# Performance work log

Hardware: AMD Instinct MI355X
Metric: run time of the kernel (lower is better)

Reference implementation:

```python
import jax, jax.numpy as jnp
import numpy as np

N_DST = 100000


def setup_inputs() -> dict:
    key = jax.random.key(0)
    ks = jax.random.split(key, 12)
    R, Ns, E, Din, H = 3, 100000, 1000000, 128, 64
    return {
        "dst_feat": jax.random.normal(ks[0], (N_DST, Din), jnp.float32),
        "neigh_feats": jax.random.normal(ks[1], (R, Ns, Din), jnp.float32),
        "Wt": jax.random.normal(ks[2], (R + 1, Din, H), jnp.float32) * 0.05,
        "bt": jnp.zeros((R + 1, H), jnp.float32),
        "attn_l": jax.random.normal(ks[3], (R, H), jnp.float32) * 0.1,
        "attn_r": jax.random.normal(ks[4], (R, H), jnp.float32) * 0.1,
        "W1": jax.random.normal(ks[5], (H, 128), jnp.float32) * 0.1,
        "b1": jnp.zeros((128,), jnp.float32),
        "w2": jax.random.normal(ks[6], (128, 1), jnp.float32) * 0.1,
        "src_idx": jax.random.randint(ks[7], (R, E), 0, Ns, jnp.int32),
        "dst_idx": jax.random.randint(ks[8], (R, E), 0, N_DST, jnp.int32),
    }


def _gat_relation(h_src, h_dst, al, ar, src, dst):
    # el/er: per-node attention logits (dot with attn vectors)
    el = h_src @ al  # [Ns]
    er = h_dst @ ar  # [Nd]
    e = jax.nn.leaky_relu(el[src] + er[dst], 0.01)  # [E]
    # edge softmax per destination node (segment softmax)
    m = jax.ops.segment_max(e, dst, num_segments=N_DST)
    a = jnp.exp(e - m[dst])
    s = jax.ops.segment_sum(a, dst, num_segments=N_DST)
    a = a / s[dst]
    # weighted aggregation: sum_e a_e * h_src[src_e]
    out = jax.ops.segment_sum(h_src[src] * a[:, None], dst, num_segments=N_DST)
    return jax.nn.elu(out)


def reference(dst_feat, neigh_feats, Wt, bt, attn_l, attn_r, W1, b1, w2, src_idx, dst_idx):
    R = neigh_feats.shape[0]
    h_dst = dst_feat @ Wt[0] + bt[0]  # weight_T[0]
    z_r = []
    for r in range(R):
        h_src = neigh_feats[r] @ Wt[r + 1] + bt[r + 1]
        z_r.append(_gat_relation(h_src, h_dst, attn_l[r], attn_r[r], src_idx[r], dst_idx[r]))
    z_r = jnp.stack(z_r, axis=1)  # [N, R, D]
    # semantic attention
    w = (jnp.tanh(z_r @ W1 + b1) @ w2).mean(axis=0)  # [R, 1]
    a_w = jax.nn.softmax(w, axis=0)  # softmax over relations
    z = (z_r * a_w[None]).sum(axis=1)  # [N, D]
    return z
```

## Files before the change

kernel.cpp:

```cpp
#include <hip/hip_runtime.h>
#include <hip/hip_fp16.h>

#define N_DST 100000
#define DIN 128
#define HDIM 64
#define RREL 3
#define NE 1000000

#define NBKT_REL 196
#define NBKT (RREL * NBKT_REL)
#define NSEG (RREL * N_DST)
#define EDGE_CHUNK 16384
#define NBLK_BIN ((RREL * NE + EDGE_CHUNK - 1) / EDGE_CHUNK)

typedef _Float16 f16x8 __attribute__((ext_vector_type(8)));
typedef float f32x4 __attribute__((ext_vector_type(4)));

__global__ __launch_bounds__(256) void k_gemm(
    const float* __restrict__ dst_feat, const float* __restrict__ neigh,
    const float* __restrict__ Wt, const float* __restrict__ bt,
    const float* __restrict__ attn_l, const float* __restrict__ attn_r,
    __half* __restrict__ h16, float* __restrict__ el, float* __restrict__ er) {
  const int RB = (N_DST + 127) / 128;
  int mat = blockIdx.x / RB;
  int row0 = (blockIdx.x % RB) * 128;
  const float* A = (mat == 0) ? dst_feat : (neigh + (size_t)(mat - 1) * N_DST * DIN);
  const float* W = Wt + (size_t)mat * DIN * HDIM;
  const float* b = bt + mat * HDIM;

  __shared__ __align__(16) unsigned char lds[48 * 1024];
  unsigned char* ldsA = lds;
  unsigned char* ldsW = lds + 32768;

  int tid = threadIdx.x;

#pragma unroll
  for (int i = 0; i < 8; i++) {
    int s = tid + 256 * i;
    int row = s >> 4;
    int kb = s & 15;
    int gr = row0 + row;
    if (gr >= N_DST) gr = N_DST - 1;
    const float* ap = A + (size_t)gr * DIN + kb * 8;
    float4 v0 = *(const float4*)ap;
    float4 v1 = *(const float4*)(ap + 4);
    f16x8 hv;
    hv[0] = (_Float16)v0.x; hv[1] = (_Float16)v0.y;
    hv[2] = (_Float16)v0.z; hv[3] = (_Float16)v0.w;
    hv[4] = (_Float16)v1.x; hv[5] = (_Float16)v1.y;
    hv[6] = (_Float16)v1.z; hv[7] = (_Float16)v1.w;
    *(f16x8*)(ldsA + row * 256 + ((kb * 16) ^ ((row & 7) << 4))) = hv;
  }

  {
    int col = tid & 63;
    int kq = tid >> 6;
    const float* wp = W + (size_t)(kq * 32) * HDIM + col;
    float wr[32];
#pragma unroll
    for (int m = 0; m < 32; m++) wr[m] = wp[(size_t)m * HDIM];
#pragma unroll
    for (int m8 = 0; m8 < 4; m8++) {
      f16x8 hv;
#pragma unroll
      for (int j = 0; j < 8; j++) hv[j] = (_Float16)wr[m8 * 8 + j];
      int byt = kq * 64 + m8 * 16;
      *(f16x8*)(ldsW + col * 256 + (byt ^ ((col & 7) << 4))) = hv;
    }
  }
  __syncthreads();

  int w = tid >> 6;
  int l = tid & 63;
  int li = l & 15;
  int hi = l >> 4;
  f32x4 acc[2][4] = {};
#pragma unroll
  for (int ks = 0; ks < 4; ks++) {
    int kbyte = ks * 64 + hi * 16;
    f16x8 af[2], bf[4];
#pragma unroll
    for (int rt = 0; rt < 2; rt++) {
      int row = w * 32 + rt * 16 + li;
      af[rt] = *(f16x8*)(ldsA + row * 256 + (kbyte ^ ((row & 7) << 4)));
    }
#pragma unroll
    for (int ct = 0; ct < 4; ct++) {
      int col = ct * 16 + li;
      bf[ct] = *(f16x8*)(ldsW + col * 256 + (kbyte ^ ((col & 7) << 4)));
    }
#pragma unroll
    for (int rt = 0; rt < 2; rt++)
#pragma unroll
      for (int ct = 0; ct < 4; ct++)
        acc[rt][ct] = __builtin_amdgcn_mfma_f32_16x16x32_f16(af[rt], bf[ct], acc[rt][ct], 0, 0, 0);
  }

  float bv[4];
#pragma unroll
  for (int ct = 0; ct < 4; ct++) bv[ct] = b[ct * 16 + li];
#pragma unroll
  for (int rt = 0; rt < 2; rt++)
#pragma unroll
    for (int ct = 0; ct < 4; ct++)
#pragma unroll
      for (int j = 0; j < 4; j++) acc[rt][ct][j] += bv[ct];

  if (mat == 0) {
#pragma unroll
    for (int r = 0; r < RREL; r++) {
      float av[4];
#pragma unroll
      for (int ct = 0; ct < 4; ct++) av[ct] = attn_r[r * HDIM + ct * 16 + li];
#pragma unroll
      for (int rt = 0; rt < 2; rt++) {
        float p[4];
#pragma unroll
        for (int j = 0; j < 4; j++)
          p[j] = acc[rt][0][j] * av[0] + acc[rt][1][j] * av[1] +
                 acc[rt][2][j] * av[2] + acc[rt][3][j] * av[3];
#pragma unroll
        for (int o = 1; o < 16; o <<= 1)
#pragma unroll
          for (int j = 0; j < 4; j++) p[j] += __shfl_xor(p[j], o);
        if (li == 0) {
#pragma unroll
          for (int j = 0; j < 4; j++) {
            int gr = row0 + w * 32 + rt * 16 + hi * 4 + j;
            if (gr < N_DST) er[r * N_DST + gr] = p[j];
          }
        }
      }
    }
  } else {
    int r = mat - 1;
    float av[4];
#pragma unroll
    for (int ct = 0; ct < 4; ct++) av[ct] = attn_l[r * HDIM + ct * 16 + li];
#pragma unroll
    for (int rt = 0; rt < 2; rt++) {
      float p[4];
#pragma unroll
      for (int j = 0; j < 4; j++)
        p[j] = acc[rt][0][j] * av[0] + acc[rt][1][j] * av[1] +
               acc[rt][2][j] * av[2] + acc[rt][3][j] * av[3];
#pragma unroll
      for (int o = 1; o < 16; o <<= 1)
#pragma unroll
        for (int j = 0; j < 4; j++) p[j] += __shfl_xor(p[j], o);
      if (li == 0) {
#pragma unroll
        for (int j = 0; j < 4; j++) {
          int gr = row0 + w * 32 + rt * 16 + hi * 4 + j;
          if (gr < N_DST) el[r * N_DST + gr] = p[j];
        }
      }
    }
    __half* hb = h16 + (size_t)r * N_DST * HDIM;
#pragma unroll
    for (int rt = 0; rt < 2; rt++)
#pragma unroll
      for (int j = 0; j < 4; j++) {
        int gr = row0 + w * 32 + rt * 16 + hi * 4 + j;
        if (gr < N_DST) {
#pragma unroll
          for (int ct = 0; ct < 4; ct++)
            hb[(size_t)gr * HDIM + ct * 16 + li] = __float2half(acc[rt][ct][j]);
        }
      }
  }
}


__global__ __launch_bounds__(256) void k_hist(const int* __restrict__ dst_idx,
                                              int* __restrict__ hist) {
  __shared__ int h[NBKT];
  int tid = threadIdx.x;
  int blk = blockIdx.x;
  for (int i = tid; i < NBKT; i += 256) h[i] = 0;
  __syncthreads();
  int e0 = blk * EDGE_CHUNK;
  int e1 = min(e0 + EDGE_CHUNK, RREL * NE);
  for (int idx = e0 + tid; idx < e1; idx += 256) {
    int r = idx / NE;
    int d = dst_idx[idx];
    atomicAdd(&h[r * NBKT_REL + (d >> 9)], 1);
  }
  __syncthreads();
  for (int i = tid; i < NBKT; i += 256)
    hist[(size_t)i * NBLK_BIN + blk] = h[i];
}

__global__ __launch_bounds__(256) void k_colscan(int* __restrict__ hist,
                                                 int* __restrict__ bcounts) {
  __shared__ int sm[256];
  int b = blockIdx.x;
  int tid = threadIdx.x;
  int v = (tid < NBLK_BIN) ? hist[(size_t)b * NBLK_BIN + tid] : 0;
  sm[tid] = v;
  __syncthreads();
  for (int off = 1; off < 256; off <<= 1) {
    int t = (tid >= off) ? sm[tid - off] : 0;
    __syncthreads();
    sm[tid] += t;
    __syncthreads();
  }
  if (tid < NBLK_BIN) hist[(size_t)b * NBLK_BIN + tid] = sm[tid] - v;
  if (tid == 255) bcounts[b] = sm[255];
}

__global__ __launch_bounds__(256) void k_bscan(const int* __restrict__ bcounts,
                                               int* __restrict__ bucket_base,
                                               int* __restrict__ offsets) {
  __shared__ int sm[256];
  int tid = threadIdx.x;
  int base = tid * 3;
  int c[3];
#pragma unroll
  for (int k = 0; k < 3; k++) c[k] = (base + k < NBKT) ? bcounts[base + k] : 0;
  int tsum = c[0] + c[1] + c[2];
  sm[tid] = tsum;
  __syncthreads();
  for (int off = 1; off < 256; off <<= 1) {
    int v = (tid >= off) ? sm[tid - off] : 0;
    __syncthreads();
    sm[tid] += v;
    __syncthreads();
  }
  int run = sm[tid] - tsum;
#pragma unroll
  for (int k = 0; k < 3; k++) {
    if (base + k < NBKT) bucket_base[base + k] = run;
    run += c[k];
  }
  if (tid == 255) bucket_base[NBKT] = sm[255];
  if (tid == 0) offsets[NSEG] = RREL * NE;
}

__global__ __launch_bounds__(256) void k_place(const int* __restrict__ src_idx,
                                               const int* __restrict__ dst_idx,
                                               const int* __restrict__ hist,
                                               const int* __restrict__ bucket_base,
                                               unsigned* __restrict__ tmp) {
  __shared__ int cur[NBKT];
  int tid = threadIdx.x;
  int blk = blockIdx.x;
  for (int i = tid; i < NBKT; i += 256)
    cur[i] = bucket_base[i] + hist[(size_t)i * NBLK_BIN + blk];
  __syncthreads();
  int e0 = blk * EDGE_CHUNK;
  int e1 = min(e0 + EDGE_CHUNK, RREL * NE);
  for (int idx = e0 + tid; idx < e1; idx += 256) {
    int r = idx / NE;
    int d = dst_idx[idx];
    int s = src_idx[idx];
    int bucket = r * NBKT_REL + (d >> 9);
    int pos = atomicAdd(&cur[bucket], 1);
    tmp[pos] = ((unsigned)(d & 511) << 17) | (unsigned)s;
  }
}

__global__ __launch_bounds__(256) void k_bucket_csr(
    const int* __restrict__ bucket_base, const unsigned* __restrict__ tmp,
    int* __restrict__ src_sorted, int* __restrict__ offsets) {
  __shared__ int cnt[512];
  __shared__ int base_l[512];
  __shared__ int sm[256];
  int b = blockIdx.x;
  int r = b / NBKT_REL;
  int brel = b - r * NBKT_REL;
  int gbase = bucket_base[b];
  int gend = bucket_base[b + 1];
  int tid = threadIdx.x;
  cnt[tid] = 0;
  cnt[tid + 256] = 0;
  __syncthreads();
  for (int e = gbase + tid; e < gend; e += 256)
    atomicAdd(&cnt[tmp[e] >> 17], 1);
  __syncthreads();
  int c0 = cnt[2 * tid], c1 = cnt[2 * tid + 1];
  int tsum = c0 + c1;
  sm[tid] = tsum;
  __syncthreads();
  for (int off = 1; off < 256; off <<= 1) {
    int v = (tid >= off) ? sm[tid - off] : 0;
    __syncthreads();
    sm[tid] += v;
    __syncthreads();
  }
  int run = sm[tid] - tsum;
  base_l[2 * tid] = run;
  base_l[2 * tid + 1] = run + c0;
  __syncthreads();
  for (int s = tid; s < 512; s += 256) {
    int dst = (brel << 9) + s;
    if (dst < N_DST) offsets[r * N_DST + dst] = gbase + base_l[s];
    cnt[s] = 0;
  }
  __syncthreads();
  for (int e = gbase + tid; e < gend; e += 256) {
    unsigned w = tmp[e];
    int s = w >> 17;
    int pos = gbase + base_l[s] + atomicAdd(&cnt[s], 1);
    src_sorted[pos] = (int)(w & 0x1FFFFu);
  }
}

__global__ __launch_bounds__(256) void k_aggregate(
    const int* __restrict__ offsets, const int* __restrict__ src_sorted,
    const float* __restrict__ el, const float* __restrict__ er,
    const __half* __restrict__ h16, float* __restrict__ zbuf) {
  int gw = blockIdx.x * 32 + (threadIdx.x >> 3);
  int li = threadIdx.x & 7;
  if (gw >= NSEG) return;
  int r = gw / N_DST;
  int start = offsets[gw], end = offsets[gw + 1];
  float erv = er[gw];
  const unsigned char* hs = (const unsigned char*)(h16 + (size_t)r * N_DST * HDIM);
  const float* elr = el + (size_t)r * N_DST;
  float acc[8] = {};
  float ssum = 0.f;
  int sNext = (start < end) ? src_sorted[start] : 0;
  for (int e = start; e < end; ++e) {
    int s = sNext;
    if (e + 1 < end) sNext = src_sorted[e + 1];
    float x = elr[s] + erv;
    float4 rv = *(const float4*)(hs + (unsigned)(s * 128 + li * 16));
    x = (x > 0.f) ? x : 0.01f * x;
    float a = __expf(x);
    ssum += a;
    const __half2* hp = (const __half2*)&rv;
#pragma unroll
    for (int q = 0; q < 4; q++) {
      float2 f = __half22float2(hp[q]);
      acc[2 * q] += a * f.x;
      acc[2 * q + 1] += a * f.y;
    }
  }
  float inv = (end > start) ? 1.f / ssum : 0.f;
  float zv[8];
#pragma unroll
  for (int q = 0; q < 8; q++) {
    float v = acc[q] * inv;
    zv[q] = (v > 0.f) ? v : (__expf(v) - 1.f);
  }
  float* zp = zbuf + (size_t)gw * HDIM + li * 8;
  *(float4*)zp = make_float4(zv[0], zv[1], zv[2], zv[3]);
  *(float4*)(zp + 4) = make_float4(zv[4], zv[5], zv[6], zv[7]);
}

__global__ __launch_bounds__(256) void k_semantic(
    const float* __restrict__ zbuf, const float* __restrict__ W1,
    const float* __restrict__ b1, const float* __restrict__ w2,
    float* __restrict__ w_acc) {
  __shared__ float W1l[64 * 128];
  __shared__ float zsh[64 * 68];
  __shared__ float wsum[RREL];
  int tid = threadIdx.x;
  if (tid < RREL) wsum[tid] = 0.f;
  for (int i = tid * 4; i < 64 * 128; i += 1024)
    *(float4*)(W1l + i) = *(const float4*)(W1 + i);
  long row0 = (long)blockIdx.x * 64;
  for (int t4 = tid; t4 < 1024; t4 += 256) {
    int rl = t4 >> 4;
    int j4 = (t4 & 15) << 2;
    long row = row0 + rl;
    float4 v = make_float4(0.f, 0.f, 0.f, 0.f);
    if (row < (long)NSEG) v = *(const float4*)(zbuf + row * HDIM + j4);
    *(float4*)(zsh + rl * 68 + j4) = v;
  }
  __syncthreads();
  int tc = tid & 31;
  int tr = tid >> 5;
  float acc[8][4] = {};
#pragma unroll 1
  for (int jj = 0; jj < 64; jj += 4) {
    float4 wv[4];
#pragma unroll
    for (int j = 0; j < 4; j++) wv[j] = *(float4*)(W1l + (jj + j) * 128 + 4 * tc);
#pragma unroll
    for (int ih = 0; ih < 2; ih++) {
      float4 zv[4];
#pragma unroll
      for (int i = 0; i < 4; i++) zv[i] = *(float4*)(zsh + (8 * tr + 4 * ih + i) * 68 + jj);
#pragma unroll
      for (int i = 0; i < 4; i++) {
        const float* zp = (const float*)&zv[i];
#pragma unroll
        for (int j = 0; j < 4; j++) {
          const float* wp = (const float*)&wv[j];
          float zz = zp[j];
#pragma unroll
          for (int c = 0; c < 4; c++) acc[4 * ih + i][c] += zz * wp[c];
        }
      }
    }
  }
  float b1v[4], w2v[4];
#pragma unroll
  for (int c = 0; c < 4; c++) {
    b1v[c] = b1[4 * tc + c];
    w2v[c] = w2[4 * tc + c];
  }
#pragma unroll
  for (int i = 0; i < 8; i++) {
    long row = row0 + 8 * tr + i;
    float p = 0.f;
#pragma unroll
    for (int c = 0; c < 4; c++) {
      float x = acc[i][c] + b1v[c];
      float ex = __expf(2.f * x);
      p += (1.f - 2.f / (ex + 1.f)) * w2v[c];
    }
#pragma unroll
    for (int o = 16; o > 0; o >>= 1) p += __shfl_xor(p, o);
    if (tc == 0 && row < (long)NSEG) {
      int r = (int)(row / N_DST);
      atomicAdd(&wsum[r], p);
    }
  }
  __syncthreads();
  if (tid < RREL) atomicAdd(&w_acc[tid], wsum[tid]);
}

__global__ __launch_bounds__(256) void k_final(const float* __restrict__ zbuf,
                                               const float* __restrict__ w_acc,
                                               float* __restrict__ out) {
  int idx = blockIdx.x * 256 + threadIdx.x;
  if (idx >= N_DST * HDIM / 4) return;
  const float invN = 1.0f / N_DST;
  float w0 = w_acc[0] * invN, w1 = w_acc[1] * invN, w2v = w_acc[2] * invN;
  float m = fmaxf(w0, fmaxf(w1, w2v));
  float e0 = __expf(w0 - m), e1 = __expf(w1 - m), e2 = __expf(w2v - m);
  float inv = 1.f / (e0 + e1 + e2);
  e0 *= inv; e1 *= inv; e2 *= inv;
  size_t o = (size_t)idx * 4;
  const size_t stride = (size_t)N_DST * HDIM;
  float4 z0 = *(const float4*)(zbuf + o);
  float4 z1 = *(const float4*)(zbuf + stride + o);
  float4 z2 = *(const float4*)(zbuf + 2 * stride + o);
  float4 r;
  r.x = e0 * z0.x + e1 * z1.x + e2 * z2.x;
  r.y = e0 * z0.y + e1 * z1.y + e2 * z2.y;
  r.z = e0 * z0.z + e1 * z1.z + e2 * z2.z;
  r.w = e0 * z0.w + e1 * z1.w + e2 * z2.w;
  *(float4*)(out + o) = r;
}

extern "C" void kernel_launch(void* const* d_in, const int* in_sizes, int n_in,
                              void* d_out, int out_size, void* d_ws, size_t ws_size,
                              hipStream_t stream) {
  const float* dst_feat = (const float*)d_in[0];
  const float* neigh = (const float*)d_in[1];
  const float* Wt = (const float*)d_in[2];
  const float* bt = (const float*)d_in[3];
  const float* attn_l = (const float*)d_in[4];
  const float* attn_r = (const float*)d_in[5];
  const float* W1 = (const float*)d_in[6];
  const float* b1 = (const float*)d_in[7];
  const float* w2 = (const float*)d_in[8];
  const int* src_idx = (const int*)d_in[9];
  const int* dst_idx = (const int*)d_in[10];
  float* out = (float*)d_out;

  char* p = (char*)d_ws;
  auto alloc = [&](size_t bytes) {
    char* q = p;
    p += (bytes + 255) & ~(size_t)255;
    return (void*)q;
  };
  __half* h16 = (__half*)alloc((size_t)RREL * N_DST * HDIM * 2);
  float* el = (float*)alloc((size_t)RREL * N_DST * 4);
  float* er = (float*)alloc((size_t)RREL * N_DST * 4);
  float* zbuf = (float*)alloc((size_t)RREL * N_DST * HDIM * 4);
  float* w_acc = (float*)alloc(64);
  int* offsets = (int*)alloc(((size_t)NSEG + 1) * 4);
  int* hist = (int*)alloc((size_t)NBKT * NBLK_BIN * 4);
  int* bcounts = (int*)alloc((size_t)NBKT * 4);
  int* bucket_base = (int*)alloc((size_t)(NBKT + 1) * 4);
  unsigned* tmp = (unsigned*)alloc((size_t)RREL * NE * 4);
  int* src_sorted = (int*)alloc((size_t)RREL * NE * 4);

  hipMemsetAsync(w_acc, 0, 64, stream);

  k_gemm<<<4 * ((N_DST + 127) / 128), 256, 0, stream>>>(dst_feat, neigh, Wt, bt, attn_l, attn_r,
                                                        h16, el, er);
  k_hist<<<NBLK_BIN, 256, 0, stream>>>(dst_idx, hist);
  k_colscan<<<NBKT, 256, 0, stream>>>(hist, bcounts);
  k_bscan<<<1, 256, 0, stream>>>(bcounts, bucket_base, offsets);
  k_place<<<NBLK_BIN, 256, 0, stream>>>(src_idx, dst_idx, hist, bucket_base, tmp);
  k_bucket_csr<<<NBKT, 256, 0, stream>>>(bucket_base, tmp, src_sorted, offsets);
  k_aggregate<<<(NSEG + 31) / 32, 256, 0, stream>>>(offsets, src_sorted, el, er, h16, zbuf);
  k_semantic<<<(NSEG + 63) / 64, 256, 0, stream>>>(zbuf, W1, b1, w2, w_acc);
  k_final<<<(N_DST * HDIM / 4 + 255) / 256, 256, 0, stream>>>(zbuf, w_acc, out);
}
```

Before: 545.9 us.

## Use fp16 MFMA for semantic-attention projection with swizzled LDS tiles

Rewrites the semantic attention kernel so the z·W1 projection runs on MFMA 16x16x32 f16 instructions instead of scalar FP32 FMAs. z rows and W1 are converted to fp16 and stored in LDS with an XOR swizzle to avoid bank conflicts. Each block now handles 128 rows, which halves the grid. The cost is reduced precision in the tanh logits that feed the relation softmax.

After: 506.1 us. 7.3% less time.

```diff
diff --git a/kernel.cpp b/kernel.cpp
--- a/kernel.cpp
+++ b/kernel.cpp
@@ -353,71 +353,103 @@
     const float* __restrict__ zbuf, const float* __restrict__ W1,
     const float* __restrict__ b1, const float* __restrict__ w2,
     float* __restrict__ w_acc) {
-  __shared__ float W1l[64 * 128];
-  __shared__ float zsh[64 * 68];
+  __shared__ __align__(16) unsigned char lds[32 * 1024];
+  unsigned char* ldsZ = lds;
+  unsigned char* ldsW = lds + 16384;
   __shared__ float wsum[RREL];
   int tid = threadIdx.x;
   if (tid < RREL) wsum[tid] = 0.f;
-  for (int i = tid * 4; i < 64 * 128; i += 1024)
-    *(float4*)(W1l + i) = *(const float4*)(W1 + i);
-  long row0 = (long)blockIdx.x * 64;
-  for (int t4 = tid; t4 < 1024; t4 += 256) {
-    int rl = t4 >> 4;
-    int j4 = (t4 & 15) << 2;
-    long row = row0 + rl;
-    float4 v = make_float4(0.f, 0.f, 0.f, 0.f);
-    if (row < (long)NSEG) v = *(const float4*)(zbuf + row * HDIM + j4);
-    *(float4*)(zsh + rl * 68 + j4) = v;
-  }
-  __syncthreads();
-  int tc = tid & 31;
-  int tr = tid >> 5;
-  float acc[8][4] = {};
-#pragma unroll 1
-  for (int jj = 0; jj < 64; jj += 4) {
-    float4 wv[4];
-#pragma unroll
-    for (int j = 0; j < 4; j++) wv[j] = *(float4*)(W1l + (jj + j) * 128 + 4 * tc);
-#pragma unroll
-    for (int ih = 0; ih < 2; ih++) {
-      float4 zv[4];
-#pragma unroll
-      for (int i = 0; i < 4; i++) zv[i] = *(float4*)(zsh + (8 * tr + 4 * ih + i) * 68 + jj);
-#pragma unroll
-      for (int i = 0; i < 4; i++) {
-        const float* zp = (const float*)&zv[i];
-#pragma unroll
-        for (int j = 0; j < 4; j++) {
-          const float* wp = (const float*)&wv[j];
-          float zz = zp[j];
-#pragma unroll
-          for (int c = 0; c < 4; c++) acc[4 * ih + i][c] += zz * wp[c];
-        }
+  int row0 = blockIdx.x * 128;
+
+  {
+    int col = tid & 127;
+    int kq = tid >> 7;
+    const float* wp = W1 + (size_t)(kq * 32) * 128 + col;
+    float wr[32];
+#pragma unroll
+    for (int m = 0; m < 32; m++) wr[m] = wp[(size_t)m * 128];
+#pragma unroll
+    for (int m8 = 0; m8 < 4; m8++) {
+      f16x8 hv;
+#pragma unroll
+      for (int j = 0; j < 8; j++) hv[j] = (_Float16)wr[m8 * 8 + j];
+      int byt = kq * 64 + m8 * 16;
+      *(f16x8*)(ldsW + col * 128 + (byt ^ ((col & 7) << 4))) = hv;
+    }
+  }
+#pragma unroll
+  for (int i = 0; i < 4; i++) {
+    int s = tid + 256 * i;
+    int row = s >> 3;
+    int kb = s & 7;
+    int gr = row0 + row;
+    if (gr >= NSEG) gr = NSEG - 1;
+    const float* zp = zbuf + (size_t)gr * HDIM + kb * 8;
+    float4 v0 = *(const float4*)zp;
+    float4 v1 = *(const float4*)(zp + 4);
+    f16x8 hv;
+    hv[0] = (_Float16)v0.x; hv[1] = (_Float16)v0.y;
+    hv[2] = (_Float16)v0.z; hv[3] = (_Float16)v0.w;
+    hv[4] = (_Float16)v1.x; hv[5] = (_Float16)v1.y;
+    hv[6] = (_Float16)v1.z; hv[7] = (_Float16)v1.w;
+    *(f16x8*)(ldsZ + row * 128 + ((kb * 16) ^ ((row & 7) << 4))) = hv;
+  }
+  __syncthreads();
+
+  int w = tid >> 6;
+  int l = tid & 63;
+  int li = l & 15;
+  int hi = l >> 4;
+  f32x4 acc[2][8] = {};
+#pragma unroll
+  for (int ks = 0; ks < 2; ks++) {
+    int kbyte = ks * 64 + hi * 16;
+    f16x8 af[2], bf[8];
+#pragma unroll
+    for (int rt = 0; rt < 2; rt++) {
+      int row = w * 32 + rt * 16 + li;
+      af[rt] = *(f16x8*)(ldsZ + row * 128 + (kbyte ^ ((row & 7) << 4)));
+    }
+#pragma unroll
+    for (int ct = 0; ct < 8; ct++) {
+      int col = ct * 16 + li;
+      bf[ct] = *(f16x8*)(ldsW + col * 128 + (kbyte ^ ((col & 7) << 4)));
+    }
+#pragma unroll
+    for (int rt = 0; rt < 2; rt++)
+#pragma unroll
+      for (int ct = 0; ct < 8; ct++)
+        acc[rt][ct] = __builtin_amdgcn_mfma_f32_16x16x32_f16(af[rt], bf[ct], acc[rt][ct], 0, 0, 0);
+  }
+
+  float p[2][4] = {};
+#pragma unroll
+  for (int ct = 0; ct < 8; ct++) {
+    float b1v = b1[ct * 16 + li];
+    float w2v = w2[ct * 16 + li];
+#pragma unroll
+    for (int rt = 0; rt < 2; rt++)
+#pragma unroll
+      for (int j = 0; j < 4; j++) {
+        float x = acc[rt][ct][j] + b1v;
+        float ex = __expf(2.f * x);
+        p[rt][j] += (1.f - 2.f / (ex + 1.f)) * w2v;
       }
-    }
-  }
-  float b1v[4], w2v[4];
-#pragma unroll
-  for (int c = 0; c < 4; c++) {
-    b1v[c] = b1[4 * tc + c];
-    w2v[c] = w2[4 * tc + c];
-  }
-#pragma unroll
-  for (int i = 0; i < 8; i++) {
-    long row = row0 + 8 * tr + i;
-    float p = 0.f;
-#pragma unroll
-    for (int c = 0; c < 4; c++) {
-      float x = acc[i][c] + b1v[c];
-      float ex = __expf(2.f * x);
-      p += (1.f - 2.f / (ex + 1.f)) * w2v[c];
-    }
-#pragma unroll
-    for (int o = 16; o > 0; o >>= 1) p += __shfl_xor(p, o);
-    if (tc == 0 && row < (long)NSEG) {
-      int r = (int)(row / N_DST);
-      atomicAdd(&wsum[r], p);
-    }
+  }
+#pragma unroll
+  for (int o = 1; o < 16; o <<= 1)
+#pragma unroll
+    for (int rt = 0; rt < 2; rt++)
+#pragma unroll
+      for (int j = 0; j < 4; j++) p[rt][j] += __shfl_xor(p[rt][j], o);
+  if (li == 0) {
+#pragma unroll
+    for (int rt = 0; rt < 2; rt++)
+#pragma unroll
+      for (int j = 0; j < 4; j++) {
+        int row = row0 + w * 32 + rt * 16 + hi * 4 + j;
+        if (row < NSEG) atomicAdd(&wsum[row / N_DST], p[rt][j]);
+      }
   }
   __syncthreads();
   if (tid < RREL) atomicAdd(&w_acc[tid], wsum[tid]);
@@ -491,6 +523,6 @@
   k_place<<<NBLK_BIN, 256, 0, stream>>>(src_idx, dst_idx, hist, bucket_base, tmp);
   k_bucket_csr<<<NBKT, 256, 0, stream>>>(bucket_base, tmp, src_sorted, offsets);
   k_aggregate<<<(NSEG + 31) / 32, 256, 0, stream>>>(offsets, src_sorted, el, er, h16, zbuf);
-  k_semantic<<<(NSEG + 63) / 64, 256, 0, stream>>>(zbuf, W1, b1, w2, w_acc);
+  k_semantic<<<(NSEG + 127) / 128, 256, 0, stream>>>(zbuf, W1, b1, w2, w_acc);
   k_final<<<(N_DST * HDIM / 4 + 255) / 256, 256, 0, stream>>>(zbuf, w_acc, out);
 }
```
